# Kernel optimization log

Hardware: AMD Instinct MI355X
Metric: run time of the kernel (lower is better)

## Reference

```python
import jax, jax.numpy as jnp
import numpy as np

B, N, D = 256, 64, 512        # batch, num_patches, dim
H, DH = 8, 64                 # heads, dim_head
INNER = H * DH                # 512
SCALE = DH ** -0.5


def setup_inputs() -> dict:
    key = jax.random.key(0)
    k0, k1, k2, k3, k4 = jax.random.split(key, 5)
    s = 0.02
    return {
        "x": jax.random.normal(k0, (B, N, D), jnp.float32),
        "Wq": jax.random.normal(k1, (D, INNER), jnp.float32) * s,      # to_q (no bias)
        "Wkv": jax.random.normal(k2, (D, 2 * INNER), jnp.float32) * s,  # to_k_v (no bias)
        "Wout": jax.random.normal(k3, (INNER, D), jnp.float32) * s,     # to_out Linear weight
        "bout": jnp.zeros((D,), jnp.float32),                           # to_out Linear bias
        "Wspec": jax.random.normal(k4, (N, 3 * N), jnp.float32) * s,    # to_qkv_spec (no bias)
    }


def reference(x, Wq, Wkv, Wout, bout, Wspec):
    b, n, d = x.shape
    # --- center-token spatial attention ---
    median_idx = n // 2
    x_center = jnp.broadcast_to(x[:, median_idx:median_idx + 1, :], (b, n, d))
    q = (x_center @ Wq).reshape(b, n, H, DH).transpose(0, 2, 1, 3)   # b h n dh
    kv = x @ Wkv                                                      # b n 2*inner
    k, v = jnp.split(kv, 2, axis=-1)
    k = k.reshape(b, n, H, DH).transpose(0, 2, 1, 3)                  # b h n dh
    v = v.reshape(b, n, H, DH).transpose(0, 2, 1, 3)                  # b h n dh
    attn = jax.nn.softmax(jnp.einsum('bhnd,bhmd->bhnm', q, k) * SCALE, axis=-1)
    out = jnp.einsum('bhnm,bhmd->bhnd', attn, v)                      # b h n dh
    out = out.transpose(0, 2, 1, 3).reshape(b, n, INNER)              # b n inner
    spatial_out = out @ Wout + bout                                   # b n d (dropout=0 -> identity)
    # --- transposed spectral attention ---
    x_t = x.transpose(0, 2, 1)                                        # b d n
    qkv = x_t @ Wspec                                                 # b d 3n
    q_s, k_s, _v_s = jnp.split(qkv, 3, axis=-1)                       # v_spec is unused in the original
    spec_weights = jax.nn.softmax(
        jnp.einsum('bdn,ben->bde', q_s, k_s) * SCALE, axis=-1)        # b d d
    # --- final combining matmul ---
    return jnp.einsum('bnd,bde->bne', spatial_out, spec_weights)      # b n d
```

## Files before the change

kernel.cpp:

```cpp
#include <hip/hip_runtime.h>

#define NP 64
#define DIM 512
#define NH 8
#define SCALE 0.125f

typedef __attribute__((ext_vector_type(4))) float f32x4;
typedef __attribute__((ext_vector_type(8))) short bf16x8;

#define WS_C   0
#define WS_MT  8192
#define WS_PT  4202496
#define WS_U   8396800
#define WS_Y   10493952

static __device__ __forceinline__ unsigned short f2bf(float f) {
  unsigned int u = __builtin_bit_cast(unsigned int, f);
  u += 0x7fffu + ((u >> 16) & 1u);
  return (unsigned short)(u >> 16);
}
static __device__ __forceinline__ float bf2f(unsigned short s) {
  return __builtin_bit_cast(float, ((unsigned int)s) << 16);
}
static __device__ __forceinline__ unsigned pk2(float a, float b) {
  return (unsigned)f2bf(a) | ((unsigned)f2bf(b) << 16);
}

__global__ __launch_bounds__(512)
void kw_prep(const float* __restrict__ Wq, const float* __restrict__ Wkv,
             const float* __restrict__ Wout, const float* __restrict__ Wspec,
             char* __restrict__ ws) {
  __shared__ float wa[64 * 65];
  __shared__ float wb[64 * 65];
  const int t = threadIdx.x;
  const int blk = blockIdx.x;
  const int sr = t >> 3, sc8 = (t & 7) * 8;

  if (blk == 1024) {
    #pragma unroll
    for (int cc = 0; cc < 8; ++cc) {
      wa[sr * 65 + sc8 + cc] = Wspec[sr * 192 + sc8 + cc];
      wb[sr * 65 + sc8 + cc] = Wspec[sr * 192 + 64 + sc8 + cc];
    }
    __syncthreads();
    const int m = sr, mm0 = sc8;
    float acc[8] = {0.f, 0.f, 0.f, 0.f, 0.f, 0.f, 0.f, 0.f};
    for (int n = 0; n < 64; ++n) {
      float qv = wa[m * 65 + n];
      #pragma unroll
      for (int j = 0; j < 8; ++j)
        acc[j] = fmaf(qv, wb[(mm0 + j) * 65 + n], acc[j]);
    }
    uint4 pk;
    pk.x = pk2(acc[0] * SCALE, acc[1] * SCALE);
    pk.y = pk2(acc[2] * SCALE, acc[3] * SCALE);
    pk.z = pk2(acc[4] * SCALE, acc[5] * SCALE);
    pk.w = pk2(acc[6] * SCALE, acc[7] * SCALE);
    *(uint4*)(ws + WS_C + m * 128 + ((mm0 * 2) ^ ((m & 7) << 4))) = pk;
    return;
  }

  const bool isP = blk >= 512;
  const int id = blk & 511;
  const int h = id >> 6, et = (id >> 3) & 7, dt = id & 7;

  const float* sa = isP ? (Wkv + (size_t)(dt * 64 + sr) * 1024 + 512 + h * 64)
                        : (Wq + (size_t)(dt * 64 + sr) * 512 + h * 64);
  const float* sb = isP ? (Wout + (size_t)(h * 64 + sr) * 512 + et * 64)
                        : (Wkv + (size_t)(et * 64 + sr) * 1024 + h * 64);
  {
    float4 a0 = *(const float4*)(sa + sc8), a1 = *(const float4*)(sa + sc8 + 4);
    float* d = wa + sr * 65 + sc8;
    d[0] = a0.x; d[1] = a0.y; d[2] = a0.z; d[3] = a0.w;
    d[4] = a1.x; d[5] = a1.y; d[6] = a1.z; d[7] = a1.w;
    float4 b0 = *(const float4*)(sb + sc8), b1 = *(const float4*)(sb + sc8 + 4);
    float* e = wb + sr * 65 + sc8;
    e[0] = b0.x; e[1] = b0.y; e[2] = b0.z; e[3] = b0.w;
    e[4] = b1.x; e[5] = b1.y; e[6] = b1.z; e[7] = b1.w;
  }
  __syncthreads();

  const int er = sr, dc8 = sc8;
  float acc[8] = {0.f, 0.f, 0.f, 0.f, 0.f, 0.f, 0.f, 0.f};
  if (!isP) {
    for (int j = 0; j < 64; ++j) {
      float bv = wb[er * 65 + j];
      #pragma unroll
      for (int dd = 0; dd < 8; ++dd)
        acc[dd] = fmaf(bv, wa[(dc8 + dd) * 65 + j], acc[dd]);
    }
  } else {
    for (int j = 0; j < 64; ++j) {
      float bv = wb[j * 65 + er];
      #pragma unroll
      for (int dd = 0; dd < 8; ++dd)
        acc[dd] = fmaf(bv, wa[(dc8 + dd) * 65 + j], acc[dd]);
    }
  }
  uint4 pk;
  pk.x = pk2(acc[0], acc[1]);
  pk.y = pk2(acc[2], acc[3]);
  pk.z = pk2(acc[4], acc[5]);
  pk.w = pk2(acc[6], acc[7]);
  if (!isP)
    *(uint4*)(ws + WS_MT + ((size_t)(h * 512 + et * 64 + er) * 512 + dt * 64 + dc8) * 2) = pk;
  else
    *(uint4*)(ws + WS_PT + ((size_t)(et * 64 + er) * 4096 + h * 512 + dt * 64 + dc8) * 2) = pk;
}

#define GEMM_LDS 131072
__global__ __launch_bounds__(512, 2)
void ku_u(const float* __restrict__ x, const char* __restrict__ ws,
          char* __restrict__ ws_u) {
  extern __shared__ char sm[];
  char* At = sm;
  char* Bt = sm + 65536;
  const int t = threadIdx.x, lane = t & 63, wave = t >> 6;
  const int bt = blockIdx.x >> 6, nt = blockIdx.x & 63;
  const int b0 = bt * 64, n0 = nt * 64;
  const char* Mt = ws + WS_MT;

  #pragma unroll
  for (int i = 0; i < 8; ++i) {
    const int r = wave * 8 + i;
    const float4* xr = (const float4*)(x + ((size_t)(b0 + r) * 64 + 32) * 512);
    float4 a = xr[lane], c = xr[64 + lane];
    uint2 pa = {pk2(a.x, a.y), pk2(a.z, a.w)};
    uint2 pc = {pk2(c.x, c.y), pk2(c.z, c.w)};
    const int swz = (r & 7) << 4;
    const int byt = (8 * (lane & 15)) ^ swz;
    *(uint2*)(At + (lane >> 4) * 8192 + r * 128 + byt) = pa;
    *(uint2*)(At + (4 + (lane >> 4)) * 8192 + r * 128 + byt) = pc;
  }
  #pragma unroll
  for (int i = 0; i < 8; ++i) {
    const int r = wave * 8 + i;
    uint4 v = ((const uint4*)(Mt + (size_t)(n0 + r) * 1024))[lane];
    *(uint4*)(Bt + (lane >> 3) * 8192 + r * 128 + ((16 * (lane & 7)) ^ ((r & 7) << 4))) = v;
  }
  __syncthreads();

  const int lo = ((lane & 15) * 128) + (((lane >> 4) * 16) ^ ((lane & 7) << 4));
  const int hi = ((lane & 15) * 128) + ((((lane >> 4) * 16) + 64) ^ ((lane & 7) << 4));
  const int bsub = wave & 3, npair = wave >> 2;

  f32x4 c0 = {0.f, 0.f, 0.f, 0.f}, c1 = {0.f, 0.f, 0.f, 0.f};
  #pragma unroll
  for (int kc = 0; kc < 8; ++kc) {
    const char* ab = At + kc * 8192 + bsub * 2048;
    bf16x8 aL = *(const bf16x8*)(ab + lo);
    bf16x8 aH = *(const bf16x8*)(ab + hi);
    const char* bb0 = Bt + kc * 8192 + (npair * 2) * 2048;
    const char* bb1 = bb0 + 2048;
    c0 = __builtin_amdgcn_mfma_f32_16x16x32_bf16(aL, *(const bf16x8*)(bb0 + lo), c0, 0, 0, 0);
    c0 = __builtin_amdgcn_mfma_f32_16x16x32_bf16(aH, *(const bf16x8*)(bb0 + hi), c0, 0, 0, 0);
    c1 = __builtin_amdgcn_mfma_f32_16x16x32_bf16(aL, *(const bf16x8*)(bb1 + lo), c1, 0, 0, 0);
    c1 = __builtin_amdgcn_mfma_f32_16x16x32_bf16(aH, *(const bf16x8*)(bb1 + hi), c1, 0, 0, 0);
  }
  unsigned short* U = (unsigned short*)ws_u;
  const int brow = b0 + bsub * 16 + (lane >> 4) * 4;
  const int nc0 = n0 + (npair * 2) * 16 + (lane & 15);
  #pragma unroll
  for (int r = 0; r < 4; ++r) {
    U[(size_t)(brow + r) * 4096 + nc0] = f2bf(c0[r]);
    U[(size_t)(brow + r) * 4096 + nc0 + 16] = f2bf(c1[r]);
  }
}

__global__ __launch_bounds__(512)
void k2_attn(const float* __restrict__ x, const char* __restrict__ ws_u,
             char* __restrict__ ws_y) {
  __shared__ float ul[8 * 512];
  __shared__ float scoreL[8 * 64];
  __shared__ float pT[64 * 8];
  const int t = threadIdx.x;
  const int lane = t & 63;
  const int wave = t >> 6;
  const int b = blockIdx.x;
  const float* xb = x + (size_t)b * NP * DIM;

  {
    uint4 v = ((const uint4*)(ws_u + (size_t)b * 8192))[t];
    const unsigned short* pv = (const unsigned short*)&v;
    float* d = ul + t * 8;
    #pragma unroll
    for (int g = 0; g < 8; ++g) d[g] = bf2f(pv[g]);
  }
  __syncthreads();

  {
    float4 uf0[8], uf1[8];
    #pragma unroll
    for (int h = 0; h < 8; ++h) {
      uf0[h] = *(const float4*)(ul + h * 512 + 4 * lane);
      uf1[h] = *(const float4*)(ul + h * 512 + 256 + 4 * lane);
    }
    #pragma unroll 2
    for (int i = 0; i < 8; ++i) {
      const int m = wave * 8 + i;
      const float4* xr = (const float4*)(xb + (size_t)m * DIM);
      float4 xv0 = xr[lane];
      float4 xv1 = xr[64 + lane];
      #pragma unroll
      for (int h = 0; h < 8; ++h) {
        float p = xv0.x * uf0[h].x + xv0.y * uf0[h].y + xv0.z * uf0[h].z + xv0.w * uf0[h].w
                + xv1.x * uf1[h].x + xv1.y * uf1[h].y + xv1.z * uf1[h].z + xv1.w * uf1[h].w;
        p += __shfl_xor(p, 1);
        p += __shfl_xor(p, 2);
        p += __shfl_xor(p, 4);
        p += __shfl_xor(p, 8);
        p += __shfl_xor(p, 16);
        p += __shfl_xor(p, 32);
        if (lane == 0) scoreL[h * 64 + m] = p;
      }
    }
  }
  __syncthreads();

  {
    float sc = scoreL[wave * 64 + lane] * SCALE;
    float mx = sc;
    #pragma unroll
    for (int off = 32; off > 0; off >>= 1)
      mx = fmaxf(mx, __shfl_xor(mx, off));
    float ev = __expf(sc - mx);
    float sm = ev;
    #pragma unroll
    for (int off = 32; off > 0; off >>= 1)
      sm += __shfl_xor(sm, off);
    pT[lane * NH + wave] = ev / sm;
  }
  __syncthreads();

  {
    float acc[NH];
    #pragma unroll
    for (int h = 0; h < NH; ++h) acc[h] = 0.f;
    #pragma unroll 2
    for (int m = 0; m < NP; ++m) {
      float xv = xb[(size_t)m * DIM + t];
      const float4* pp = (const float4*)(pT + m * NH);
      float4 p0 = pp[0], p1 = pp[1];
      acc[0] = fmaf(p0.x, xv, acc[0]);
      acc[1] = fmaf(p0.y, xv, acc[1]);
      acc[2] = fmaf(p0.z, xv, acc[2]);
      acc[3] = fmaf(p0.w, xv, acc[3]);
      acc[4] = fmaf(p1.x, xv, acc[4]);
      acc[5] = fmaf(p1.y, xv, acc[5]);
      acc[6] = fmaf(p1.z, xv, acc[6]);
      acc[7] = fmaf(p1.w, xv, acc[7]);
    }
    unsigned short* Y = (unsigned short*)ws_y;
    #pragma unroll
    for (int h = 0; h < NH; ++h)
      Y[(size_t)b * 4096 + h * 512 + t] = f2bf(acc[h]);
  }
}

__global__ __launch_bounds__(512, 2)
void ks_s(const char* __restrict__ ws_y, const char* __restrict__ ws_pt,
          float* __restrict__ Spart) {
  extern __shared__ char sm[];
  char* At = sm;
  char* Bt = sm + 65536;
  const int t = threadIdx.x, lane = t & 63, wave = t >> 6;
  const int bt = blockIdx.x >> 6, et = (blockIdx.x >> 3) & 7, sl = blockIdx.x & 7;
  const int b0 = bt * 64, e0 = et * 64;
  const size_t kb2 = (size_t)sl * 1024;

  #pragma unroll
  for (int i = 0; i < 8; ++i) {
    const int r = wave * 8 + i;
    const int byt = (16 * (lane & 7)) ^ ((r & 7) << 4);
    uint4 va = ((const uint4*)(ws_y + (size_t)(b0 + r) * 8192 + kb2))[lane];
    *(uint4*)(At + (lane >> 3) * 8192 + r * 128 + byt) = va;
    uint4 vb = ((const uint4*)(ws_pt + (size_t)(e0 + r) * 8192 + kb2))[lane];
    *(uint4*)(Bt + (lane >> 3) * 8192 + r * 128 + byt) = vb;
  }
  __syncthreads();

  const int lo = ((lane & 15) * 128) + (((lane >> 4) * 16) ^ ((lane & 7) << 4));
  const int hi = ((lane & 15) * 128) + ((((lane >> 4) * 16) + 64) ^ ((lane & 7) << 4));
  const int bsub = wave & 3, epair = wave >> 2;

  f32x4 c0 = {0.f, 0.f, 0.f, 0.f}, c1 = {0.f, 0.f, 0.f, 0.f};
  #pragma unroll
  for (int kc = 0; kc < 8; ++kc) {
    const char* ab = At + kc * 8192 + bsub * 2048;
    bf16x8 aL = *(const bf16x8*)(ab + lo);
    bf16x8 aH = *(const bf16x8*)(ab + hi);
    const char* bb0 = Bt + kc * 8192 + (epair * 2) * 2048;
    const char* bb1 = bb0 + 2048;
    c0 = __builtin_amdgcn_mfma_f32_16x16x32_bf16(aL, *(const bf16x8*)(bb0 + lo), c0, 0, 0, 0);
    c0 = __builtin_amdgcn_mfma_f32_16x16x32_bf16(aH, *(const bf16x8*)(bb0 + hi), c0, 0, 0, 0);
    c1 = __builtin_amdgcn_mfma_f32_16x16x32_bf16(aL, *(const bf16x8*)(bb1 + lo), c1, 0, 0, 0);
    c1 = __builtin_amdgcn_mfma_f32_16x16x32_bf16(aH, *(const bf16x8*)(bb1 + hi), c1, 0, 0, 0);
  }
  const int brow = b0 + bsub * 16 + (lane >> 4) * 4;
  const int ec0 = e0 + (epair * 2) * 16 + (lane & 15);
  #pragma unroll
  for (int r = 0; r < 4; ++r) {
    Spart[((size_t)sl * 256 + brow + r) * 512 + ec0] = c0[r];
    Spart[((size_t)sl * 256 + brow + r) * 512 + ec0 + 16] = c1[r];
  }
}

#define K4_LDS 142336
__global__ __launch_bounds__(512)
void k4_spec(const float* __restrict__ x, const char* __restrict__ Cws,
             const float* __restrict__ Spart, const float* __restrict__ bout,
             float* __restrict__ out) {
  extern __shared__ char smem[];
  char* xTc  = smem;
  char* w2Tc = smem + 65536;
  char* Cc   = smem + 131072;
  float* s_l = (float*)(smem + 139264);
  float* rsx = (float*)(smem + 141312);

  const int t = threadIdx.x;
  const int lane = t & 63;
  const int wave = t >> 6;
  const int b = blockIdx.x;
  const float* xb = x + (size_t)b * NP * DIM;

  const int lo_off = ((lane & 15) * 128) + ((((lane >> 4) * 16)) ^ ((lane & 7) << 4));
  const int hi_off = ((lane & 15) * 128) + ((((lane >> 4) * 16) + 64) ^ ((lane & 7) << 4));

  {
    const int d = t;
    #pragma unroll
    for (int c = 0; c < 8; ++c) {
      float v0 = xb[(c * 8 + 0) * DIM + d];
      float v1 = xb[(c * 8 + 1) * DIM + d];
      float v2 = xb[(c * 8 + 2) * DIM + d];
      float v3 = xb[(c * 8 + 3) * DIM + d];
      float v4 = xb[(c * 8 + 4) * DIM + d];
      float v5 = xb[(c * 8 + 5) * DIM + d];
      float v6 = xb[(c * 8 + 6) * DIM + d];
      float v7 = xb[(c * 8 + 7) * DIM + d];
      uint4 pk;
      pk.x = pk2(v0, v1);
      pk.y = pk2(v2, v3);
      pk.z = pk2(v4, v5);
      pk.w = pk2(v6, v7);
      *(uint4*)(xTc + d * 128 + ((c * 16) ^ ((d & 7) << 4))) = pk;
    }
    ((uint4*)Cc)[t] = ((const uint4*)Cws)[t];
    float sacc = bout[t];
    #pragma unroll
    for (int sl = 0; sl < 8; ++sl)
      sacc += Spart[((size_t)sl * 256 + b) * 512 + t];
    s_l[t] = sacc;
  }
  __syncthreads();

  {
    bf16x8 af0[4], af1[4];
    #pragma unroll
    for (int mt = 0; mt < 4; ++mt) {
      af0[mt] = *(const bf16x8*)(Cc + mt * 16 * 128 + lo_off);
      af1[mt] = *(const bf16x8*)(Cc + mt * 16 * 128 + hi_off);
    }
    #pragma unroll
    for (int etl = 0; etl < 4; ++etl) {
      const int e0 = (wave * 4 + etl) * 16;
      bf16x8 b0 = *(const bf16x8*)(xTc + e0 * 128 + lo_off);
      bf16x8 b1 = *(const bf16x8*)(xTc + e0 * 128 + hi_off);
      const int e = e0 + (lane & 15);
      #pragma unroll
      for (int mt = 0; mt < 4; ++mt) {
        f32x4 c = {0.f, 0.f, 0.f, 0.f};
        c = __builtin_amdgcn_mfma_f32_16x16x32_bf16(af0[mt], b0, c, 0, 0, 0);
        c = __builtin_amdgcn_mfma_f32_16x16x32_bf16(af1[mt], b1, c, 0, 0, 0);
        const int mrow = mt * 16 + (lane >> 4) * 4;
        uint2 pk;
        pk.x = pk2(c[0], c[1]);
        pk.y = pk2(c[2], c[3]);
        *(uint2*)(w2Tc + e * 128 + ((mrow * 2) ^ ((e & 7) << 4))) = pk;
      }
    }
  }
  __syncthreads();

  const int dslot = wave & 3, ehalf = wave >> 2;
  const int rowg = (lane >> 4) * 4;
  float treg[16];
  #pragma unroll
  for (int i = 0; i < 16; ++i) treg[i] = 0.f;

  #pragma unroll 1
  for (int pass = 0; pass < 8; ++pass) {
    const int d0 = (pass * 4 + dslot) * 16;
    bf16x8 a0 = *(const bf16x8*)(xTc + d0 * 128 + lo_off);
    bf16x8 a1 = *(const bf16x8*)(xTc + d0 * 128 + hi_off);

    float rs[4] = {0.f, 0.f, 0.f, 0.f};
    uint2 pex[16];
    #pragma unroll
    for (int i = 0; i < 16; ++i) {
      const int et = ehalf * 16 + i;
      bf16x8 b0 = *(const bf16x8*)(w2Tc + et * 2048 + lo_off);
      bf16x8 b1 = *(const bf16x8*)(w2Tc + et * 2048 + hi_off);
      f32x4 c = {0.f, 0.f, 0.f, 0.f};
      c = __builtin_amdgcn_mfma_f32_16x16x32_bf16(a0, b0, c, 0, 0, 0);
      c = __builtin_amdgcn_mfma_f32_16x16x32_bf16(a1, b1, c, 0, 0, 0);
      uint2 p;
      p.x = pk2(__expf(c[0]), __expf(c[1]));
      p.y = pk2(__expf(c[2]), __expf(c[3]));
      pex[i] = p;
      rs[0] += bf2f((unsigned short)(p.x & 0xffffu));
      rs[1] += bf2f((unsigned short)(p.x >> 16));
      rs[2] += bf2f((unsigned short)(p.y & 0xffffu));
      rs[3] += bf2f((unsigned short)(p.y >> 16));
    }
    #pragma unroll
    for (int r = 0; r < 4; ++r) {
      rs[r] += __shfl_xor(rs[r], 1);
      rs[r] += __shfl_xor(rs[r], 2);
      rs[r] += __shfl_xor(rs[r], 4);
      rs[r] += __shfl_xor(rs[r], 8);
    }
    const int pb = pass & 1;
    if ((lane & 15) == 0) {
      #pragma unroll
      for (int r = 0; r < 4; ++r)
        rsx[pb * 128 + wave * 16 + rowg + r] = rs[r];
    }
    __syncthreads();
    float coef[4];
    #pragma unroll
    for (int r = 0; r < 4; ++r) {
      const float rfull = rsx[pb * 128 + wave * 16 + rowg + r]
                        + rsx[pb * 128 + (wave ^ 4) * 16 + rowg + r];
      coef[r] = s_l[d0 + rowg + r] / rfull;
    }
    #pragma unroll
    for (int i = 0; i < 16; ++i) {
      uint2 p = pex[i];
      float tp = treg[i];
      tp = fmaf(coef[0], bf2f((unsigned short)(p.x & 0xffffu)), tp);
      tp = fmaf(coef[1], bf2f((unsigned short)(p.x >> 16)), tp);
      tp = fmaf(coef[2], bf2f((unsigned short)(p.y & 0xffffu)), tp);
      tp = fmaf(coef[3], bf2f((unsigned short)(p.y >> 16)), tp);
      treg[i] = tp;
    }
  }

  #pragma unroll
  for (int i = 0; i < 16; ++i) {
    treg[i] += __shfl_xor(treg[i], 16);
    treg[i] += __shfl_xor(treg[i], 32);
  }
  float* wpart = (float*)xTc;
  if (lane < 16) {
    #pragma unroll
    for (int i = 0; i < 16; ++i)
      wpart[dslot * 512 + ehalf * 256 + i * 16 + lane] = treg[i];
  }
  __syncthreads();

  float tf = 0.f;
  #pragma unroll
  for (int w = 0; w < 4; ++w) tf += wpart[w * 512 + t];

  float* ob = out + (size_t)b * NP * DIM + t;
  #pragma unroll 4
  for (int n = 0; n < NP; ++n) ob[n * DIM] = tf;
}

extern "C" void kernel_launch(void* const* d_in, const int* in_sizes, int n_in,
                              void* d_out, int out_size, void* d_ws, size_t ws_size,
                              hipStream_t stream) {
  (void)in_sizes; (void)n_in; (void)out_size; (void)ws_size;
  const float* x     = (const float*)d_in[0];
  const float* Wq    = (const float*)d_in[1];
  const float* Wkv   = (const float*)d_in[2];
  const float* Wout  = (const float*)d_in[3];
  const float* bout  = (const float*)d_in[4];
  const float* Wspec = (const float*)d_in[5];
  float* out = (float*)d_out;

  char* ws = (char*)d_ws;

  hipFuncSetAttribute(reinterpret_cast<const void*>(ku_u),
                      hipFuncAttributeMaxDynamicSharedMemorySize, GEMM_LDS);
  hipFuncSetAttribute(reinterpret_cast<const void*>(ks_s),
                      hipFuncAttributeMaxDynamicSharedMemorySize, GEMM_LDS);
  hipFuncSetAttribute(reinterpret_cast<const void*>(k4_spec),
                      hipFuncAttributeMaxDynamicSharedMemorySize, K4_LDS);

  kw_prep<<<dim3(1025), dim3(512), 0, stream>>>(Wq, Wkv, Wout, Wspec, ws);
  ku_u   <<<dim3(256),  dim3(512), GEMM_LDS, stream>>>(x, ws, ws + WS_U);
  k2_attn<<<dim3(256),  dim3(512), 0, stream>>>(x, ws + WS_U, ws + WS_Y);
  ks_s   <<<dim3(256),  dim3(512), GEMM_LDS, stream>>>(ws + WS_Y, ws + WS_PT,
                                                       (float*)(ws + WS_MT));
  k4_spec<<<dim3(256),  dim3(512), K4_LDS, stream>>>(x, ws, (const float*)(ws + WS_MT),
                                                     bout, out);
}
```

Before: 108.0 us.

## Fuse five kernels into one cooperative kernel with grid syncs

Replaces the five separate launches (weight prep, U GEMM, attention, S GEMM, spectral) with a single cooperative mega-kernel of 256 blocks that separates the stages with grid.sync(). The weight-prep stage's 1025 blocks become a grid-stride loop. The aim is to remove inter-kernel launch gaps and tail effects. In exchange it adds grid-wide barrier overhead and forces every stage to run at 142KB LDS and one block per CU, which may lower occupancy for the GEMM stages that previously ran with launch bound 2.

```diff
diff --git a/kernel.cpp b/kernel.cpp
--- a/kernel.cpp
+++ b/kernel.cpp
@@ -1,4 +1,7 @@
 #include <hip/hip_runtime.h>
+#include <hip/hip_cooperative_groups.h>
+
+namespace cg = cooperative_groups;
 
 #define NP 64
 #define DIM 512
@@ -13,6 +16,8 @@
 #define WS_PT  4202496
 #define WS_U   8396800
 #define WS_Y   10493952
+
+#define MEGA_LDS 142336
 
 static __device__ __forceinline__ unsigned short f2bf(float f) {
   unsigned int u = __builtin_bit_cast(unsigned int, f);
@@ -27,445 +32,436 @@
 }
 
 __global__ __launch_bounds__(512)
-void kw_prep(const float* __restrict__ Wq, const float* __restrict__ Wkv,
-             const float* __restrict__ Wout, const float* __restrict__ Wspec,
-             char* __restrict__ ws) {
-  __shared__ float wa[64 * 65];
-  __shared__ float wb[64 * 65];
-  const int t = threadIdx.x;
-  const int blk = blockIdx.x;
-  const int sr = t >> 3, sc8 = (t & 7) * 8;
-
-  if (blk == 1024) {
-    #pragma unroll
-    for (int cc = 0; cc < 8; ++cc) {
-      wa[sr * 65 + sc8 + cc] = Wspec[sr * 192 + sc8 + cc];
-      wb[sr * 65 + sc8 + cc] = Wspec[sr * 192 + 64 + sc8 + cc];
-    }
-    __syncthreads();
-    const int m = sr, mm0 = sc8;
-    float acc[8] = {0.f, 0.f, 0.f, 0.f, 0.f, 0.f, 0.f, 0.f};
-    for (int n = 0; n < 64; ++n) {
-      float qv = wa[m * 65 + n];
-      #pragma unroll
-      for (int j = 0; j < 8; ++j)
-        acc[j] = fmaf(qv, wb[(mm0 + j) * 65 + n], acc[j]);
-    }
-    uint4 pk;
-    pk.x = pk2(acc[0] * SCALE, acc[1] * SCALE);
-    pk.y = pk2(acc[2] * SCALE, acc[3] * SCALE);
-    pk.z = pk2(acc[4] * SCALE, acc[5] * SCALE);
-    pk.w = pk2(acc[6] * SCALE, acc[7] * SCALE);
-    *(uint4*)(ws + WS_C + m * 128 + ((mm0 * 2) ^ ((m & 7) << 4))) = pk;
-    return;
-  }
-
-  const bool isP = blk >= 512;
-  const int id = blk & 511;
-  const int h = id >> 6, et = (id >> 3) & 7, dt = id & 7;
-
-  const float* sa = isP ? (Wkv + (size_t)(dt * 64 + sr) * 1024 + 512 + h * 64)
-                        : (Wq + (size_t)(dt * 64 + sr) * 512 + h * 64);
-  const float* sb = isP ? (Wout + (size_t)(h * 64 + sr) * 512 + et * 64)
-                        : (Wkv + (size_t)(et * 64 + sr) * 1024 + h * 64);
-  {
-    float4 a0 = *(const float4*)(sa + sc8), a1 = *(const float4*)(sa + sc8 + 4);
-    float* d = wa + sr * 65 + sc8;
-    d[0] = a0.x; d[1] = a0.y; d[2] = a0.z; d[3] = a0.w;
-    d[4] = a1.x; d[5] = a1.y; d[6] = a1.z; d[7] = a1.w;
-    float4 b0 = *(const float4*)(sb + sc8), b1 = *(const float4*)(sb + sc8 + 4);
-    float* e = wb + sr * 65 + sc8;
-    e[0] = b0.x; e[1] = b0.y; e[2] = b0.z; e[3] = b0.w;
-    e[4] = b1.x; e[5] = b1.y; e[6] = b1.z; e[7] = b1.w;
-  }
-  __syncthreads();
-
-  const int er = sr, dc8 = sc8;
-  float acc[8] = {0.f, 0.f, 0.f, 0.f, 0.f, 0.f, 0.f, 0.f};
-  if (!isP) {
-    for (int j = 0; j < 64; ++j) {
-      float bv = wb[er * 65 + j];
-      #pragma unroll
-      for (int dd = 0; dd < 8; ++dd)
-        acc[dd] = fmaf(bv, wa[(dc8 + dd) * 65 + j], acc[dd]);
-    }
-  } else {
-    for (int j = 0; j < 64; ++j) {
-      float bv = wb[j * 65 + er];
-      #pragma unroll
-      for (int dd = 0; dd < 8; ++dd)
-        acc[dd] = fmaf(bv, wa[(dc8 + dd) * 65 + j], acc[dd]);
-    }
-  }
-  uint4 pk;
-  pk.x = pk2(acc[0], acc[1]);
-  pk.y = pk2(acc[2], acc[3]);
-  pk.z = pk2(acc[4], acc[5]);
-  pk.w = pk2(acc[6], acc[7]);
-  if (!isP)
-    *(uint4*)(ws + WS_MT + ((size_t)(h * 512 + et * 64 + er) * 512 + dt * 64 + dc8) * 2) = pk;
-  else
-    *(uint4*)(ws + WS_PT + ((size_t)(et * 64 + er) * 4096 + h * 512 + dt * 64 + dc8) * 2) = pk;
-}
-
-#define GEMM_LDS 131072
-__global__ __launch_bounds__(512, 2)
-void ku_u(const float* __restrict__ x, const char* __restrict__ ws,
-          char* __restrict__ ws_u) {
-  extern __shared__ char sm[];
-  char* At = sm;
-  char* Bt = sm + 65536;
-  const int t = threadIdx.x, lane = t & 63, wave = t >> 6;
-  const int bt = blockIdx.x >> 6, nt = blockIdx.x & 63;
-  const int b0 = bt * 64, n0 = nt * 64;
-  const char* Mt = ws + WS_MT;
-
-  #pragma unroll
-  for (int i = 0; i < 8; ++i) {
-    const int r = wave * 8 + i;
-    const float4* xr = (const float4*)(x + ((size_t)(b0 + r) * 64 + 32) * 512);
-    float4 a = xr[lane], c = xr[64 + lane];
-    uint2 pa = {pk2(a.x, a.y), pk2(a.z, a.w)};
-    uint2 pc = {pk2(c.x, c.y), pk2(c.z, c.w)};
-    const int swz = (r & 7) << 4;
-    const int byt = (8 * (lane & 15)) ^ swz;
-    *(uint2*)(At + (lane >> 4) * 8192 + r * 128 + byt) = pa;
-    *(uint2*)(At + (4 + (lane >> 4)) * 8192 + r * 128 + byt) = pc;
-  }
-  #pragma unroll
-  for (int i = 0; i < 8; ++i) {
-    const int r = wave * 8 + i;
-    uint4 v = ((const uint4*)(Mt + (size_t)(n0 + r) * 1024))[lane];
-    *(uint4*)(Bt + (lane >> 3) * 8192 + r * 128 + ((16 * (lane & 7)) ^ ((r & 7) << 4))) = v;
-  }
-  __syncthreads();
-
-  const int lo = ((lane & 15) * 128) + (((lane >> 4) * 16) ^ ((lane & 7) << 4));
-  const int hi = ((lane & 15) * 128) + ((((lane >> 4) * 16) + 64) ^ ((lane & 7) << 4));
-  const int bsub = wave & 3, npair = wave >> 2;
-
-  f32x4 c0 = {0.f, 0.f, 0.f, 0.f}, c1 = {0.f, 0.f, 0.f, 0.f};
-  #pragma unroll
-  for (int kc = 0; kc < 8; ++kc) {
-    const char* ab = At + kc * 8192 + bsub * 2048;
-    bf16x8 aL = *(const bf16x8*)(ab + lo);
-    bf16x8 aH = *(const bf16x8*)(ab + hi);
-    const char* bb0 = Bt + kc * 8192 + (npair * 2) * 2048;
-    const char* bb1 = bb0 + 2048;
-    c0 = __builtin_amdgcn_mfma_f32_16x16x32_bf16(aL, *(const bf16x8*)(bb0 + lo), c0, 0, 0, 0);
-    c0 = __builtin_amdgcn_mfma_f32_16x16x32_bf16(aH, *(const bf16x8*)(bb0 + hi), c0, 0, 0, 0);
-    c1 = __builtin_amdgcn_mfma_f32_16x16x32_bf16(aL, *(const bf16x8*)(bb1 + lo), c1, 0, 0, 0);
-    c1 = __builtin_amdgcn_mfma_f32_16x16x32_bf16(aH, *(const bf16x8*)(bb1 + hi), c1, 0, 0, 0);
-  }
-  unsigned short* U = (unsigned short*)ws_u;
-  const int brow = b0 + bsub * 16 + (lane >> 4) * 4;
-  const int nc0 = n0 + (npair * 2) * 16 + (lane & 15);
-  #pragma unroll
-  for (int r = 0; r < 4; ++r) {
-    U[(size_t)(brow + r) * 4096 + nc0] = f2bf(c0[r]);
-    U[(size_t)(brow + r) * 4096 + nc0 + 16] = f2bf(c1[r]);
-  }
-}
-
-__global__ __launch_bounds__(512)
-void k2_attn(const float* __restrict__ x, const char* __restrict__ ws_u,
-             char* __restrict__ ws_y) {
-  __shared__ float ul[8 * 512];
-  __shared__ float scoreL[8 * 64];
-  __shared__ float pT[64 * 8];
+void mega_kernel(const float* __restrict__ x, const float* __restrict__ Wq,
+                 const float* __restrict__ Wkv, const float* __restrict__ Wout,
+                 const float* __restrict__ bout, const float* __restrict__ Wspec,
+                 char* __restrict__ ws, float* __restrict__ out) {
+  extern __shared__ char smem[];
+  cg::grid_group grid = cg::this_grid();
+
   const int t = threadIdx.x;
   const int lane = t & 63;
   const int wave = t >> 6;
-  const int b = blockIdx.x;
-  const float* xb = x + (size_t)b * NP * DIM;
-
-  {
-    uint4 v = ((const uint4*)(ws_u + (size_t)b * 8192))[t];
-    const unsigned short* pv = (const unsigned short*)&v;
-    float* d = ul + t * 8;
-    #pragma unroll
-    for (int g = 0; g < 8; ++g) d[g] = bf2f(pv[g]);
-  }
-  __syncthreads();
-
-  {
-    float4 uf0[8], uf1[8];
-    #pragma unroll
-    for (int h = 0; h < 8; ++h) {
-      uf0[h] = *(const float4*)(ul + h * 512 + 4 * lane);
-      uf1[h] = *(const float4*)(ul + h * 512 + 256 + 4 * lane);
-    }
-    #pragma unroll 2
-    for (int i = 0; i < 8; ++i) {
-      const int m = wave * 8 + i;
-      const float4* xr = (const float4*)(xb + (size_t)m * DIM);
-      float4 xv0 = xr[lane];
-      float4 xv1 = xr[64 + lane];
-      #pragma unroll
-      for (int h = 0; h < 8; ++h) {
-        float p = xv0.x * uf0[h].x + xv0.y * uf0[h].y + xv0.z * uf0[h].z + xv0.w * uf0[h].w
-                + xv1.x * uf1[h].x + xv1.y * uf1[h].y + xv1.z * uf1[h].z + xv1.w * uf1[h].w;
-        p += __shfl_xor(p, 1);
-        p += __shfl_xor(p, 2);
-        p += __shfl_xor(p, 4);
-        p += __shfl_xor(p, 8);
-        p += __shfl_xor(p, 16);
-        p += __shfl_xor(p, 32);
-        if (lane == 0) scoreL[h * 64 + m] = p;
-      }
-    }
-  }
-  __syncthreads();
-
-  {
-    float sc = scoreL[wave * 64 + lane] * SCALE;
-    float mx = sc;
-    #pragma unroll
-    for (int off = 32; off > 0; off >>= 1)
-      mx = fmaxf(mx, __shfl_xor(mx, off));
-    float ev = __expf(sc - mx);
-    float sm = ev;
-    #pragma unroll
-    for (int off = 32; off > 0; off >>= 1)
-      sm += __shfl_xor(sm, off);
-    pT[lane * NH + wave] = ev / sm;
-  }
-  __syncthreads();
-
-  {
-    float acc[NH];
-    #pragma unroll
-    for (int h = 0; h < NH; ++h) acc[h] = 0.f;
-    #pragma unroll 2
-    for (int m = 0; m < NP; ++m) {
-      float xv = xb[(size_t)m * DIM + t];
-      const float4* pp = (const float4*)(pT + m * NH);
-      float4 p0 = pp[0], p1 = pp[1];
-      acc[0] = fmaf(p0.x, xv, acc[0]);
-      acc[1] = fmaf(p0.y, xv, acc[1]);
-      acc[2] = fmaf(p0.z, xv, acc[2]);
-      acc[3] = fmaf(p0.w, xv, acc[3]);
-      acc[4] = fmaf(p1.x, xv, acc[4]);
-      acc[5] = fmaf(p1.y, xv, acc[5]);
-      acc[6] = fmaf(p1.z, xv, acc[6]);
-      acc[7] = fmaf(p1.w, xv, acc[7]);
-    }
-    unsigned short* Y = (unsigned short*)ws_y;
-    #pragma unroll
-    for (int h = 0; h < NH; ++h)
-      Y[(size_t)b * 4096 + h * 512 + t] = f2bf(acc[h]);
-  }
-}
-
-__global__ __launch_bounds__(512, 2)
-void ks_s(const char* __restrict__ ws_y, const char* __restrict__ ws_pt,
-          float* __restrict__ Spart) {
-  extern __shared__ char sm[];
-  char* At = sm;
-  char* Bt = sm + 65536;
-  const int t = threadIdx.x, lane = t & 63, wave = t >> 6;
-  const int bt = blockIdx.x >> 6, et = (blockIdx.x >> 3) & 7, sl = blockIdx.x & 7;
-  const int b0 = bt * 64, e0 = et * 64;
-  const size_t kb2 = (size_t)sl * 1024;
-
-  #pragma unroll
-  for (int i = 0; i < 8; ++i) {
-    const int r = wave * 8 + i;
-    const int byt = (16 * (lane & 7)) ^ ((r & 7) << 4);
-    uint4 va = ((const uint4*)(ws_y + (size_t)(b0 + r) * 8192 + kb2))[lane];
-    *(uint4*)(At + (lane >> 3) * 8192 + r * 128 + byt) = va;
-    uint4 vb = ((const uint4*)(ws_pt + (size_t)(e0 + r) * 8192 + kb2))[lane];
-    *(uint4*)(Bt + (lane >> 3) * 8192 + r * 128 + byt) = vb;
-  }
-  __syncthreads();
-
-  const int lo = ((lane & 15) * 128) + (((lane >> 4) * 16) ^ ((lane & 7) << 4));
-  const int hi = ((lane & 15) * 128) + ((((lane >> 4) * 16) + 64) ^ ((lane & 7) << 4));
-  const int bsub = wave & 3, epair = wave >> 2;
-
-  f32x4 c0 = {0.f, 0.f, 0.f, 0.f}, c1 = {0.f, 0.f, 0.f, 0.f};
-  #pragma unroll
-  for (int kc = 0; kc < 8; ++kc) {
-    const char* ab = At + kc * 8192 + bsub * 2048;
-    bf16x8 aL = *(const bf16x8*)(ab + lo);
-    bf16x8 aH = *(const bf16x8*)(ab + hi);
-    const char* bb0 = Bt + kc * 8192 + (epair * 2) * 2048;
-    const char* bb1 = bb0 + 2048;
-    c0 = __builtin_amdgcn_mfma_f32_16x16x32_bf16(aL, *(const bf16x8*)(bb0 + lo), c0, 0, 0, 0);
-    c0 = __builtin_amdgcn_mfma_f32_16x16x32_bf16(aH, *(const bf16x8*)(bb0 + hi), c0, 0, 0, 0);
-    c1 = __builtin_amdgcn_mfma_f32_16x16x32_bf16(aL, *(const bf16x8*)(bb1 + lo), c1, 0, 0, 0);
-    c1 = __builtin_amdgcn_mfma_f32_16x16x32_bf16(aH, *(const bf16x8*)(bb1 + hi), c1, 0, 0, 0);
-  }
-  const int brow = b0 + bsub * 16 + (lane >> 4) * 4;
-  const int ec0 = e0 + (epair * 2) * 16 + (lane & 15);
-  #pragma unroll
-  for (int r = 0; r < 4; ++r) {
-    Spart[((size_t)sl * 256 + brow + r) * 512 + ec0] = c0[r];
-    Spart[((size_t)sl * 256 + brow + r) * 512 + ec0 + 16] = c1[r];
-  }
-}
-
-#define K4_LDS 142336
-__global__ __launch_bounds__(512)
-void k4_spec(const float* __restrict__ x, const char* __restrict__ Cws,
-             const float* __restrict__ Spart, const float* __restrict__ bout,
-             float* __restrict__ out) {
-  extern __shared__ char smem[];
-  char* xTc  = smem;
-  char* w2Tc = smem + 65536;
-  char* Cc   = smem + 131072;
-  float* s_l = (float*)(smem + 139264);
-  float* rsx = (float*)(smem + 141312);
-
-  const int t = threadIdx.x;
-  const int lane = t & 63;
-  const int wave = t >> 6;
-  const int b = blockIdx.x;
-  const float* xb = x + (size_t)b * NP * DIM;
+  const int bid = blockIdx.x;
 
   const int lo_off = ((lane & 15) * 128) + ((((lane >> 4) * 16)) ^ ((lane & 7) << 4));
   const int hi_off = ((lane & 15) * 128) + ((((lane >> 4) * 16) + 64) ^ ((lane & 7) << 4));
 
   {
-    const int d = t;
-    #pragma unroll
-    for (int c = 0; c < 8; ++c) {
-      float v0 = xb[(c * 8 + 0) * DIM + d];
-      float v1 = xb[(c * 8 + 1) * DIM + d];
-      float v2 = xb[(c * 8 + 2) * DIM + d];
-      float v3 = xb[(c * 8 + 3) * DIM + d];
-      float v4 = xb[(c * 8 + 4) * DIM + d];
-      float v5 = xb[(c * 8 + 5) * DIM + d];
-      float v6 = xb[(c * 8 + 6) * DIM + d];
-      float v7 = xb[(c * 8 + 7) * DIM + d];
-      uint4 pk;
-      pk.x = pk2(v0, v1);
-      pk.y = pk2(v2, v3);
-      pk.z = pk2(v4, v5);
-      pk.w = pk2(v6, v7);
-      *(uint4*)(xTc + d * 128 + ((c * 16) ^ ((d & 7) << 4))) = pk;
-    }
-    ((uint4*)Cc)[t] = ((const uint4*)Cws)[t];
-    float sacc = bout[t];
-    #pragma unroll
-    for (int sl = 0; sl < 8; ++sl)
-      sacc += Spart[((size_t)sl * 256 + b) * 512 + t];
-    s_l[t] = sacc;
+    float* wa = (float*)smem;
+    float* wb = (float*)(smem + 16640);
+    const int sr = t >> 3, sc8 = (t & 7) * 8;
+
+    for (int blk = bid; blk < 1025; blk += 256) {
+      if (blk == 1024) {
+        #pragma unroll
+        for (int cc = 0; cc < 8; ++cc) {
+          wa[sr * 65 + sc8 + cc] = Wspec[sr * 192 + sc8 + cc];
+          wb[sr * 65 + sc8 + cc] = Wspec[sr * 192 + 64 + sc8 + cc];
+        }
+        __syncthreads();
+        const int m = sr, mm0 = sc8;
+        float acc[8] = {0.f, 0.f, 0.f, 0.f, 0.f, 0.f, 0.f, 0.f};
+        for (int n = 0; n < 64; ++n) {
+          float qv = wa[m * 65 + n];
+          #pragma unroll
+          for (int j = 0; j < 8; ++j)
+            acc[j] = fmaf(qv, wb[(mm0 + j) * 65 + n], acc[j]);
+        }
+        uint4 pk;
+        pk.x = pk2(acc[0] * SCALE, acc[1] * SCALE);
+        pk.y = pk2(acc[2] * SCALE, acc[3] * SCALE);
+        pk.z = pk2(acc[4] * SCALE, acc[5] * SCALE);
+        pk.w = pk2(acc[6] * SCALE, acc[7] * SCALE);
+        *(uint4*)(ws + WS_C + m * 128 + ((mm0 * 2) ^ ((m & 7) << 4))) = pk;
+      } else {
+        const bool isP = blk >= 512;
+        const int id = blk & 511;
+        const int h = id >> 6, et = (id >> 3) & 7, dt = id & 7;
+
+        const float* sa = isP ? (Wkv + (size_t)(dt * 64 + sr) * 1024 + 512 + h * 64)
+                              : (Wq + (size_t)(dt * 64 + sr) * 512 + h * 64);
+        const float* sb = isP ? (Wout + (size_t)(h * 64 + sr) * 512 + et * 64)
+                              : (Wkv + (size_t)(et * 64 + sr) * 1024 + h * 64);
+        {
+          float4 a0 = *(const float4*)(sa + sc8), a1 = *(const float4*)(sa + sc8 + 4);
+          float* d = wa + sr * 65 + sc8;
+          d[0] = a0.x; d[1] = a0.y; d[2] = a0.z; d[3] = a0.w;
+          d[4] = a1.x; d[5] = a1.y; d[6] = a1.z; d[7] = a1.w;
+          float4 b0 = *(const float4*)(sb + sc8), b1 = *(const float4*)(sb + sc8 + 4);
+          float* e = wb + sr * 65 + sc8;
+          e[0] = b0.x; e[1] = b0.y; e[2] = b0.z; e[3] = b0.w;
+          e[4] = b1.x; e[5] = b1.y; e[6] = b1.z; e[7] = b1.w;
+        }
+        __syncthreads();
+
+        const int er = sr, dc8 = sc8;
+        float acc[8] = {0.f, 0.f, 0.f, 0.f, 0.f, 0.f, 0.f, 0.f};
+        if (!isP) {
+          for (int j = 0; j < 64; ++j) {
+            float bv = wb[er * 65 + j];
+            #pragma unroll
+            for (int dd = 0; dd < 8; ++dd)
+              acc[dd] = fmaf(bv, wa[(dc8 + dd) * 65 + j], acc[dd]);
+          }
+        } else {
+          for (int j = 0; j < 64; ++j) {
+            float bv = wb[j * 65 + er];
+            #pragma unroll
+            for (int dd = 0; dd < 8; ++dd)
+              acc[dd] = fmaf(bv, wa[(dc8 + dd) * 65 + j], acc[dd]);
+          }
+        }
+        uint4 pk;
+        pk.x = pk2(acc[0], acc[1]);
+        pk.y = pk2(acc[2], acc[3]);
+        pk.z = pk2(acc[4], acc[5]);
+        pk.w = pk2(acc[6], acc[7]);
+        if (!isP)
+          *(uint4*)(ws + WS_MT + ((size_t)(h * 512 + et * 64 + er) * 512 + dt * 64 + dc8) * 2) = pk;
+        else
+          *(uint4*)(ws + WS_PT + ((size_t)(et * 64 + er) * 4096 + h * 512 + dt * 64 + dc8) * 2) = pk;
+      }
+      __syncthreads();
+    }
   }
-  __syncthreads();
+  grid.sync();
 
   {
-    bf16x8 af0[4], af1[4];
-    #pragma unroll
-    for (int mt = 0; mt < 4; ++mt) {
-      af0[mt] = *(const bf16x8*)(Cc + mt * 16 * 128 + lo_off);
-      af1[mt] = *(const bf16x8*)(Cc + mt * 16 * 128 + hi_off);
-    }
-    #pragma unroll
-    for (int etl = 0; etl < 4; ++etl) {
-      const int e0 = (wave * 4 + etl) * 16;
-      bf16x8 b0 = *(const bf16x8*)(xTc + e0 * 128 + lo_off);
-      bf16x8 b1 = *(const bf16x8*)(xTc + e0 * 128 + hi_off);
-      const int e = e0 + (lane & 15);
+    char* At = smem;
+    char* Bt = smem + 65536;
+    const int bt = bid >> 6, nt = bid & 63;
+    const int b0 = bt * 64, n0 = nt * 64;
+    const char* Mt = ws + WS_MT;
+
+    #pragma unroll
+    for (int i = 0; i < 8; ++i) {
+      const int r = wave * 8 + i;
+      const float4* xr = (const float4*)(x + ((size_t)(b0 + r) * 64 + 32) * 512);
+      float4 a = xr[lane], c = xr[64 + lane];
+      uint2 pa = {pk2(a.x, a.y), pk2(a.z, a.w)};
+      uint2 pc = {pk2(c.x, c.y), pk2(c.z, c.w)};
+      const int swz = (r & 7) << 4;
+      const int byt = (8 * (lane & 15)) ^ swz;
+      *(uint2*)(At + (lane >> 4) * 8192 + r * 128 + byt) = pa;
+      *(uint2*)(At + (4 + (lane >> 4)) * 8192 + r * 128 + byt) = pc;
+    }
+    #pragma unroll
+    for (int i = 0; i < 8; ++i) {
+      const int r = wave * 8 + i;
+      uint4 v = ((const uint4*)(Mt + (size_t)(n0 + r) * 1024))[lane];
+      *(uint4*)(Bt + (lane >> 3) * 8192 + r * 128 + ((16 * (lane & 7)) ^ ((r & 7) << 4))) = v;
+    }
+    __syncthreads();
+
+    const int bsub = wave & 3, npair = wave >> 2;
+    f32x4 c0 = {0.f, 0.f, 0.f, 0.f}, c1 = {0.f, 0.f, 0.f, 0.f};
+    #pragma unroll
+    for (int kc = 0; kc < 8; ++kc) {
+      const char* ab = At + kc * 8192 + bsub * 2048;
+      bf16x8 aL = *(const bf16x8*)(ab + lo_off);
+      bf16x8 aH = *(const bf16x8*)(ab + hi_off);
+      const char* bb0 = Bt + kc * 8192 + (npair * 2) * 2048;
+      const char* bb1 = bb0 + 2048;
+      c0 = __builtin_amdgcn_mfma_f32_16x16x32_bf16(aL, *(const bf16x8*)(bb0 + lo_off), c0, 0, 0, 0);
+      c0 = __builtin_amdgcn_mfma_f32_16x16x32_bf16(aH, *(const bf16x8*)(bb0 + hi_off), c0, 0, 0, 0);
+      c1 = __builtin_amdgcn_mfma_f32_16x16x32_bf16(aL, *(const bf16x8*)(bb1 + lo_off), c1, 0, 0, 0);
+      c1 = __builtin_amdgcn_mfma_f32_16x16x32_bf16(aH, *(const bf16x8*)(bb1 + hi_off), c1, 0, 0, 0);
+    }
+    unsigned short* U = (unsigned short*)(ws + WS_U);
+    const int brow = b0 + bsub * 16 + (lane >> 4) * 4;
+    const int nc0 = n0 + (npair * 2) * 16 + (lane & 15);
+    #pragma unroll
+    for (int r = 0; r < 4; ++r) {
+      U[(size_t)(brow + r) * 4096 + nc0] = f2bf(c0[r]);
+      U[(size_t)(brow + r) * 4096 + nc0 + 16] = f2bf(c1[r]);
+    }
+  }
+  grid.sync();
+
+  {
+    float* ul = (float*)smem;
+    float* scoreL = (float*)(smem + 16384);
+    float* pT = (float*)(smem + 18432);
+    const int b = bid;
+    const float* xb = x + (size_t)b * NP * DIM;
+    const char* ws_u = ws + WS_U;
+
+    {
+      uint4 v = ((const uint4*)(ws_u + (size_t)b * 8192))[t];
+      const unsigned short* pv = (const unsigned short*)&v;
+      float* d = ul + t * 8;
+      #pragma unroll
+      for (int g = 0; g < 8; ++g) d[g] = bf2f(pv[g]);
+    }
+    __syncthreads();
+
+    {
+      float4 uf0[8], uf1[8];
+      #pragma unroll
+      for (int h = 0; h < 8; ++h) {
+        uf0[h] = *(const float4*)(ul + h * 512 + 4 * lane);
+        uf1[h] = *(const float4*)(ul + h * 512 + 256 + 4 * lane);
+      }
+      #pragma unroll 2
+      for (int i = 0; i < 8; ++i) {
+        const int m = wave * 8 + i;
+        const float4* xr = (const float4*)(xb + (size_t)m * DIM);
+        float4 xv0 = xr[lane];
+        float4 xv1 = xr[64 + lane];
+        #pragma unroll
+        for (int h = 0; h < 8; ++h) {
+          float p = xv0.x * uf0[h].x + xv0.y * uf0[h].y + xv0.z * uf0[h].z + xv0.w * uf0[h].w
+                  + xv1.x * uf1[h].x + xv1.y * uf1[h].y + xv1.z * uf1[h].z + xv1.w * uf1[h].w;
+          p += __shfl_xor(p, 1);
+          p += __shfl_xor(p, 2);
+          p += __shfl_xor(p, 4);
+          p += __shfl_xor(p, 8);
+          p += __shfl_xor(p, 16);
+          p += __shfl_xor(p, 32);
+          if (lane == 0) scoreL[h * 64 + m] = p;
+        }
+      }
+    }
+    __syncthreads();
+
+    {
+      float sc = scoreL[wave * 64 + lane] * SCALE;
+      float mx = sc;
+      #pragma unroll
+      for (int off = 32; off > 0; off >>= 1)
+        mx = fmaxf(mx, __shfl_xor(mx, off));
+      float ev = __expf(sc - mx);
+      float sm = ev;
+      #pragma unroll
+      for (int off = 32; off > 0; off >>= 1)
+        sm += __shfl_xor(sm, off);
+      pT[lane * NH + wave] = ev / sm;
+    }
+    __syncthreads();
+
+    {
+      float acc[NH];
+      #pragma unroll
+      for (int h = 0; h < NH; ++h) acc[h] = 0.f;
+      #pragma unroll 2
+      for (int m = 0; m < NP; ++m) {
+        float xv = xb[(size_t)m * DIM + t];
+        const float4* pp = (const float4*)(pT + m * NH);
+        float4 p0 = pp[0], p1 = pp[1];
+        acc[0] = fmaf(p0.x, xv, acc[0]);
+        acc[1] = fmaf(p0.y, xv, acc[1]);
+        acc[2] = fmaf(p0.z, xv, acc[2]);
+        acc[3] = fmaf(p0.w, xv, acc[3]);
+        acc[4] = fmaf(p1.x, xv, acc[4]);
+        acc[5] = fmaf(p1.y, xv, acc[5]);
+        acc[6] = fmaf(p1.z, xv, acc[6]);
+        acc[7] = fmaf(p1.w, xv, acc[7]);
+      }
+      unsigned short* Y = (unsigned short*)(ws + WS_Y);
+      #pragma unroll
+      for (int h = 0; h < NH; ++h)
+        Y[(size_t)b * 4096 + h * 512 + t] = f2bf(acc[h]);
+    }
+  }
+  grid.sync();
+
+  {
+    char* At = smem;
+    char* Bt = smem + 65536;
+    const int bt = bid >> 6, et = (bid >> 3) & 7, sl = bid & 7;
+    const int b0 = bt * 64, e0 = et * 64;
+    const size_t kb2 = (size_t)sl * 1024;
+    const char* ws_y = ws + WS_Y;
+    const char* ws_pt = ws + WS_PT;
+    float* Spart = (float*)(ws + WS_MT);
+
+    #pragma unroll
+    for (int i = 0; i < 8; ++i) {
+      const int r = wave * 8 + i;
+      const int byt = (16 * (lane & 7)) ^ ((r & 7) << 4);
+      uint4 va = ((const uint4*)(ws_y + (size_t)(b0 + r) * 8192 + kb2))[lane];
+      *(uint4*)(At + (lane >> 3) * 8192 + r * 128 + byt) = va;
+      uint4 vb = ((const uint4*)(ws_pt + (size_t)(e0 + r) * 8192 + kb2))[lane];
+      *(uint4*)(Bt + (lane >> 3) * 8192 + r * 128 + byt) = vb;
+    }
+    __syncthreads();
+
+    const int bsub = wave & 3, epair = wave >> 2;
+    f32x4 c0 = {0.f, 0.f, 0.f, 0.f}, c1 = {0.f, 0.f, 0.f, 0.f};
+    #pragma unroll
+    for (int kc = 0; kc < 8; ++kc) {
+      const char* ab = At + kc * 8192 + bsub * 2048;
+      bf16x8 aL = *(const bf16x8*)(ab + lo_off);
+      bf16x8 aH = *(const bf16x8*)(ab + hi_off);
+      const char* bb0 = Bt + kc * 8192 + (epair * 2) * 2048;
+      const char* bb1 = bb0 + 2048;
+      c0 = __builtin_amdgcn_mfma_f32_16x16x32_bf16(aL, *(const bf16x8*)(bb0 + lo_off), c0, 0, 0, 0);
+      c0 = __builtin_amdgcn_mfma_f32_16x16x32_bf16(aH, *(const bf16x8*)(bb0 + hi_off), c0, 0, 0, 0);
+      c1 = __builtin_amdgcn_mfma_f32_16x16x32_bf16(aL, *(const bf16x8*)(bb1 + lo_off), c1, 0, 0, 0);
+      c1 = __builtin_amdgcn_mfma_f32_16x16x32_bf16(aH, *(const bf16x8*)(bb1 + hi_off), c1, 0, 0, 0);
+    }
+    const int brow = b0 + bsub * 16 + (lane >> 4) * 4;
+    const int ec0 = e0 + (epair * 2) * 16 + (lane & 15);
+    #pragma unroll
+    for (int r = 0; r < 4; ++r) {
+      Spart[((size_t)sl * 256 + brow + r) * 512 + ec0] = c0[r];
+      Spart[((size_t)sl * 256 + brow + r) * 512 + ec0 + 16] = c1[r];
+    }
+  }
+  grid.sync();
+
+  {
+    char* xTc  = smem;
+    char* w2Tc = smem + 65536;
+    char* Cc   = smem + 131072;
+    float* s_l = (float*)(smem + 139264);
+    float* rsx = (float*)(smem + 141312);
+    const int b = bid;
+    const float* xb = x + (size_t)b * NP * DIM;
+    const float* Spart = (const float*)(ws + WS_MT);
+
+    {
+      const int d = t;
+      #pragma unroll
+      for (int c = 0; c < 8; ++c) {
+        float v0 = xb[(c * 8 + 0) * DIM + d];
+        float v1 = xb[(c * 8 + 1) * DIM + d];
+        float v2 = xb[(c * 8 + 2) * DIM + d];
+        float v3 = xb[(c * 8 + 3) * DIM + d];
+        float v4 = xb[(c * 8 + 4) * DIM + d];
+        float v5 = xb[(c * 8 + 5) * DIM + d];
+        float v6 = xb[(c * 8 + 6) * DIM + d];
+        float v7 = xb[(c * 8 + 7) * DIM + d];
+        uint4 pk;
+        pk.x = pk2(v0, v1);
+        pk.y = pk2(v2, v3);
+        pk.z = pk2(v4, v5);
+        pk.w = pk2(v6, v7);
+        *(uint4*)(xTc + d * 128 + ((c * 16) ^ ((d & 7) << 4))) = pk;
+      }
+      ((uint4*)Cc)[t] = ((const uint4*)(ws + WS_C))[t];
+      float sacc = bout[t];
+      #pragma unroll
+      for (int sl = 0; sl < 8; ++sl)
+        sacc += Spart[((size_t)sl * 256 + b) * 512 + t];
+      s_l[t] = sacc;
+    }
+    __syncthreads();
+
+    {
+      bf16x8 af0[4], af1[4];
       #pragma unroll
       for (int mt = 0; mt < 4; ++mt) {
+        af0[mt] = *(const bf16x8*)(Cc + mt * 16 * 128 + lo_off);
+        af1[mt] = *(const bf16x8*)(Cc + mt * 16 * 128 + hi_off);
+      }
+      #pragma unroll
+      for (int etl = 0; etl < 4; ++etl) {
+        const int e0 = (wave * 4 + etl) * 16;
+        bf16x8 b0 = *(const bf16x8*)(xTc + e0 * 128 + lo_off);
+        bf16x8 b1 = *(const bf16x8*)(xTc + e0 * 128 + hi_off);
+        const int e = e0 + (lane & 15);
+        #pragma unroll
+        for (int mt = 0; mt < 4; ++mt) {
+          f32x4 c = {0.f, 0.f, 0.f, 0.f};
+          c = __builtin_amdgcn_mfma_f32_16x16x32_bf16(af0[mt], b0, c, 0, 0, 0);
+          c = __builtin_amdgcn_mfma_f32_16x16x32_bf16(af1[mt], b1, c, 0, 0, 0);
+          const int mrow = mt * 16 + (lane >> 4) * 4;
+          uint2 pk;
+          pk.x = pk2(c[0], c[1]);
+          pk.y = pk2(c[2], c[3]);
+          *(uint2*)(w2Tc + e * 128 + ((mrow * 2) ^ ((e & 7) << 4))) = pk;
+        }
+      }
+    }
+    __syncthreads();
+
+    const int dslot = wave & 3, ehalf = wave >> 2;
+    const int rowg = (lane >> 4) * 4;
+    float treg[16];
+    #pragma unroll
+    for (int i = 0; i < 16; ++i) treg[i] = 0.f;
+
+    #pragma unroll 1
+    for (int pass = 0; pass < 8; ++pass) {
+      const int d0 = (pass * 4 + dslot) * 16;
+      bf16x8 a0 = *(const bf16x8*)(xTc + d0 * 128 + lo_off);
+      bf16x8 a1 = *(const bf16x8*)(xTc + d0 * 128 + hi_off);
+
+      float rs[4] = {0.f, 0.f, 0.f, 0.f};
+      uint2 pex[16];
+      #pragma unroll
+      for (int i = 0; i < 16; ++i) {
+        const int et = ehalf * 16 + i;
+        bf16x8 b0 = *(const bf16x8*)(w2Tc + et * 2048 + lo_off);
+        bf16x8 b1 = *(const bf16x8*)(w2Tc + et * 2048 + hi_off);
         f32x4 c = {0.f, 0.f, 0.f, 0.f};
-        c = __builtin_amdgcn_mfma_f32_16x16x32_bf16(af0[mt], b0, c, 0, 0, 0);
-        c = __builtin_amdgcn_mfma_f32_16x16x32_bf16(af1[mt], b1, c, 0, 0, 0);
-        const int mrow = mt * 16 + (lane >> 4) * 4;
-        uint2 pk;
-        pk.x = pk2(c[0], c[1]);
-        pk.y = pk2(c[2], c[3]);
-        *(uint2*)(w2Tc + e * 128 + ((mrow * 2) ^ ((e & 7) << 4))) = pk;
-      }
-    }
+        c = __builtin_amdgcn_mfma_f32_16x16x32_bf16(a0, b0, c, 0, 0, 0);
+        c = __builtin_amdgcn_mfma_f32_16x16x32_bf16(a1, b1, c, 0, 0, 0);
+        uint2 p;
+        p.x = pk2(__expf(c[0]), __expf(c[1]));
+        p.y = pk2(__expf(c[2]), __expf(c[3]));
+        pex[i] = p;
+        rs[0] += bf2f((unsigned short)(p.x & 0xffffu));
+        rs[1] += bf2f((unsigned short)(p.x >> 16));
+        rs[2] += bf2f((unsigned short)(p.y & 0xffffu));
+        rs[3] += bf2f((unsigned short)(p.y >> 16));
+      }
+      #pragma unroll
+      for (int r = 0; r < 4; ++r) {
+        rs[r] += __shfl_xor(rs[r], 1);
+        rs[r] += __shfl_xor(rs[r], 2);
+        rs[r] += __shfl_xor(rs[r], 4);
+        rs[r] += __shfl_xor(rs[r], 8);
+      }
+      const int pb = pass & 1;
+      if ((lane & 15) == 0) {
+        #pragma unroll
+        for (int r = 0; r < 4; ++r)
+          rsx[pb * 128 + wave * 16 + rowg + r] = rs[r];
+      }
+      __syncthreads();
+      float coef[4];
+      #pragma unroll
+      for (int r = 0; r < 4; ++r) {
+        const float rfull = rsx[pb * 128 + wave * 16 + rowg + r]
+                          + rsx[pb * 128 + (wave ^ 4) * 16 + rowg + r];
+        coef[r] = s_l[d0 + rowg + r] / rfull;
+      }
+      #pragma unroll
+      for (int i = 0; i < 16; ++i) {
+        uint2 p = pex[i];
+        float tp = treg[i];
+        tp = fmaf(coef[0], bf2f((unsigned short)(p.x & 0xffffu)), tp);
+        tp = fmaf(coef[1], bf2f((unsigned short)(p.x >> 16)), tp);
+        tp = fmaf(coef[2], bf2f((unsigned short)(p.y & 0xffffu)), tp);
+        tp = fmaf(coef[3], bf2f((unsigned short)(p.y >> 16)), tp);
+        treg[i] = tp;
+      }
+    }
+
+    #pragma unroll
+    for (int i = 0; i < 16; ++i) {
+      treg[i] += __shfl_xor(treg[i], 16);
+      treg[i] += __shfl_xor(treg[i], 32);
+    }
+    float* wpart = (float*)xTc;
+    if (lane < 16) {
+      #pragma unroll
+      for (int i = 0; i < 16; ++i)
+        wpart[dslot * 512 + ehalf * 256 + i * 16 + lane] = treg[i];
+    }
+    __syncthreads();
+
+    float tf = 0.f;
+    #pragma unroll
+    for (int w = 0; w < 4; ++w) tf += wpart[w * 512 + t];
+
+    float* ob = out + (size_t)b * NP * DIM + t;
+    #pragma unroll 4
+    for (int n = 0; n < NP; ++n) ob[n * DIM] = tf;
   }
-  __syncthreads();
-
-  const int dslot = wave & 3, ehalf = wave >> 2;
-  const int rowg = (lane >> 4) * 4;
-  float treg[16];
-  #pragma unroll
-  for (int i = 0; i < 16; ++i) treg[i] = 0.f;
-
-  #pragma unroll 1
-  for (int pass = 0; pass < 8; ++pass) {
-    const int d0 = (pass * 4 + dslot) * 16;
-    bf16x8 a0 = *(const bf16x8*)(xTc + d0 * 128 + lo_off);
-    bf16x8 a1 = *(const bf16x8*)(xTc + d0 * 128 + hi_off);
-
-    float rs[4] = {0.f, 0.f, 0.f, 0.f};
-    uint2 pex[16];
-    #pragma unroll
-    for (int i = 0; i < 16; ++i) {
-      const int et = ehalf * 16 + i;
-      bf16x8 b0 = *(const bf16x8*)(w2Tc + et * 2048 + lo_off);
-      bf16x8 b1 = *(const bf16x8*)(w2Tc + et * 2048 + hi_off);
-      f32x4 c = {0.f, 0.f, 0.f, 0.f};
-      c = __builtin_amdgcn_mfma_f32_16x16x32_bf16(a0, b0, c, 0, 0, 0);
-      c = __builtin_amdgcn_mfma_f32_16x16x32_bf16(a1, b1, c, 0, 0, 0);
-      uint2 p;
-      p.x = pk2(__expf(c[0]), __expf(c[1]));
-      p.y = pk2(__expf(c[2]), __expf(c[3]));
-      pex[i] = p;
-      rs[0] += bf2f((unsigned short)(p.x & 0xffffu));
-      rs[1] += bf2f((unsigned short)(p.x >> 16));
-      rs[2] += bf2f((unsigned short)(p.y & 0xffffu));
-      rs[3] += bf2f((unsigned short)(p.y >> 16));
-    }
-    #pragma unroll
-    for (int r = 0; r < 4; ++r) {
-      rs[r] += __shfl_xor(rs[r], 1);
-      rs[r] += __shfl_xor(rs[r], 2);
-      rs[r] += __shfl_xor(rs[r], 4);
-      rs[r] += __shfl_xor(rs[r], 8);
-    }
-    const int pb = pass & 1;
-    if ((lane & 15) == 0) {
-      #pragma unroll
-      for (int r = 0; r < 4; ++r)
-        rsx[pb * 128 + wave * 16 + rowg + r] = rs[r];
-    }
-    __syncthreads();
-    float coef[4];
-    #pragma unroll
-    for (int r = 0; r < 4; ++r) {
-      const float rfull = rsx[pb * 128 + wave * 16 + rowg + r]
-                        + rsx[pb * 128 + (wave ^ 4) * 16 + rowg + r];
-      coef[r] = s_l[d0 + rowg + r] / rfull;
-    }
-    #pragma unroll
-    for (int i = 0; i < 16; ++i) {
-      uint2 p = pex[i];
-      float tp = treg[i];
-      tp = fmaf(coef[0], bf2f((unsigned short)(p.x & 0xffffu)), tp);
-      tp = fmaf(coef[1], bf2f((unsigned short)(p.x >> 16)), tp);
-      tp = fmaf(coef[2], bf2f((unsigned short)(p.y & 0xffffu)), tp);
-      tp = fmaf(coef[3], bf2f((unsigned short)(p.y >> 16)), tp);
-      treg[i] = tp;
-    }
-  }
-
-  #pragma unroll
-  for (int i = 0; i < 16; ++i) {
-    treg[i] += __shfl_xor(treg[i], 16);
-    treg[i] += __shfl_xor(treg[i], 32);
-  }
-  float* wpart = (float*)xTc;
-  if (lane < 16) {
-    #pragma unroll
-    for (int i = 0; i < 16; ++i)
-      wpart[dslot * 512 + ehalf * 256 + i * 16 + lane] = treg[i];
-  }
-  __syncthreads();
-
-  float tf = 0.f;
-  #pragma unroll
-  for (int w = 0; w < 4; ++w) tf += wpart[w * 512 + t];
-
-  float* ob = out + (size_t)b * NP * DIM + t;
-  #pragma unroll 4
-  for (int n = 0; n < NP; ++n) ob[n * DIM] = tf;
 }
 
 extern "C" void kernel_launch(void* const* d_in, const int* in_sizes, int n_in,
@@ -478,22 +474,14 @@
   const float* Wout  = (const float*)d_in[3];
   const float* bout  = (const float*)d_in[4];
   const float* Wspec = (const float*)d_in[5];
-  float* out = (float*)d_out;
-
+  float* outp = (float*)d_out;
   char* ws = (char*)d_ws;
 
-  hipFuncSetAttribute(reinterpret_cast<const void*>(ku_u),
-                      hipFuncAttributeMaxDynamicSharedMemorySize, GEMM_LDS);
-  hipFuncSetAttribute(reinterpret_cast<const void*>(ks_s),
-                      hipFuncAttributeMaxDynamicSharedMemorySize, GEMM_LDS);
-  hipFuncSetAttribute(reinterpret_cast<const void*>(k4_spec),
-                      hipFuncAttributeMaxDynamicSharedMemorySize, K4_LDS);
-
-  kw_prep<<<dim3(1025), dim3(512), 0, stream>>>(Wq, Wkv, Wout, Wspec, ws);
-  ku_u   <<<dim3(256),  dim3(512), GEMM_LDS, stream>>>(x, ws, ws + WS_U);
-  k2_attn<<<dim3(256),  dim3(512), 0, stream>>>(x, ws + WS_U, ws + WS_Y);
-  ks_s   <<<dim3(256),  dim3(512), GEMM_LDS, stream>>>(ws + WS_Y, ws + WS_PT,
-                                                       (float*)(ws + WS_MT));
-  k4_spec<<<dim3(256),  dim3(512), K4_LDS, stream>>>(x, ws, (const float*)(ws + WS_MT),
-                                                     bout, out);
+  hipFuncSetAttribute(reinterpret_cast<const void*>(mega_kernel),
+                      hipFuncAttributeMaxDynamicSharedMemorySize, MEGA_LDS);
+
+  void* args[] = {(void*)&x, (void*)&Wq, (void*)&Wkv, (void*)&Wout,
+                  (void*)&bout, (void*)&Wspec, (void*)&ws, (void*)&outp};
+  hipLaunchCooperativeKernel(reinterpret_cast<const void*>(mega_kernel),
+                             dim3(256), dim3(512), args, MEGA_LDS, stream);
 }
```

Result: slower. 238.9 us (+121.3%).
